# Kernel optimization log

Hardware: AMD Instinct MI355X
Metric: run time of the kernel (lower is better)

Reference implementation:

```python
import jax, jax.numpy as jnp
import numpy as np

D, H, DK, L, FF = 512, 8, 64, 6, 2048
MAXREL = 512
R = 2 * MAXREL + 1
B, S = 4, 512


def _ln(x, g, b):
    m = jnp.mean(x, -1, keepdims=True)
    v = jnp.mean((x - m) ** 2, -1, keepdims=True)
    return (x - m) * jax.lax.rsqrt(v + 1e-5) * g + b


def _gelu(x):
    return jax.nn.gelu(x, approximate=False)


def setup_inputs() -> dict:
    key = jax.random.key(0)
    ks = iter(jax.random.split(key, 64))
    def rnd(shape, scale=0.02):
        return jax.random.normal(next(ks), shape, jnp.float32) * scale
    inp = {"x": jax.random.normal(next(ks), (B, S, D), jnp.float32)}
    # SeasonalDecomposition params (3 seasonal nets stacked on leading axis)
    inp.update(
        sd_t1_w=rnd((D, D)), sd_t1_b=jnp.zeros((D,), jnp.float32),
        sd_t2_w=rnd((D, D)), sd_t2_b=jnp.zeros((D,), jnp.float32),
        sd_s1_w=rnd((3, D, D // 2)), sd_s1_b=jnp.zeros((3, D // 2), jnp.float32),
        sd_s2_w=rnd((3, D // 2, D)), sd_s2_b=jnp.zeros((3, D), jnp.float32),
        sd_r1_w=rnd((D, D // 2)), sd_r1_b=jnp.zeros((D // 2,), jnp.float32),
        sd_r2_w=rnd((D // 2, D)), sd_r2_b=jnp.zeros((D,), jnp.float32),
        sd_comb=jnp.ones((5,), jnp.float32),
        # 6 TemporalFusionTransformer layers, params stacked on leading axis L
        wq=rnd((L, D, D)), wk=rnd((L, D, D)), wv=rnd((L, D, D)),
        wo_w=rnd((L, D, D)), wo_b=jnp.zeros((L, D), jnp.float32),
        rel_k=rnd((L, R, DK), 1.0), rel_v=rnd((L, R, DK), 1.0),
        ln_attn_g=jnp.ones((L, D), jnp.float32), ln_attn_b=jnp.zeros((L, D), jnp.float32),
        ff1_w=rnd((L, D, FF)), ff1_b=jnp.zeros((L, FF), jnp.float32),
        ff2_w=rnd((L, FF, D)), ff2_b=jnp.zeros((L, D), jnp.float32),
        n1_g=jnp.ones((L, D), jnp.float32), n1_b=jnp.zeros((L, D), jnp.float32),
        n2_g=jnp.ones((L, D), jnp.float32), n2_b=jnp.zeros((L, D), jnp.float32),
    )
    return inp


def _forward(x, sd_t1_w, sd_t1_b, sd_t2_w, sd_t2_b, sd_s1_w, sd_s1_b, sd_s2_w, sd_s2_b,
             sd_r1_w, sd_r1_b, sd_r2_w, sd_r2_b, sd_comb,
             wq, wk, wv, wo_w, wo_b, rel_k, rel_v, ln_attn_g, ln_attn_b,
             ff1_w, ff1_b, ff2_w, ff2_b, n1_g, n1_b, n2_g, n2_b):
    b, s, d = x.shape
    # relative position index matrix, rp[i, j] = clip(j - i) + MAXREL
    r = jnp.arange(s)
    rp = jnp.clip(r[None, :] - r[:, None], -MAXREL, MAXREL) + MAXREL  # [S, S]

    # ---- SeasonalDecomposition (eval mode: dropout = identity) ----
    trend = _gelu(x @ sd_t1_w + sd_t1_b) @ sd_t2_w + sd_t2_b
    h = _gelu(jnp.einsum('bsd,kdm->kbsm', x, sd_s1_w) + sd_s1_b[:, None, None, :])
    seas = jnp.einsum('kbsm,kmd->kbsd', h, sd_s2_w) + sd_s2_b[:, None, None, :]  # [3,B,S,D]
    resid = _gelu(x @ sd_r1_w + sd_r1_b) @ sd_r2_w + sd_r2_b
    w = jax.nn.softmax(sd_comb)
    x = w[0] * trend + w[4] * resid + jnp.einsum('k,kbsd->bsd', w[1:4], seas)

    scale = np.float32(1.0 / np.sqrt(DK))

    def layer(xc, p):
        q = (xc @ p['wq']).reshape(b, s, H, DK).transpose(0, 2, 1, 3)  # [B,H,S,DK]
        k = (xc @ p['wk']).reshape(b, s, H, DK).transpose(0, 2, 1, 3)
        v = (xc @ p['wv']).reshape(b, s, H, DK).transpose(0, 2, 1, 3)
        scores = jnp.einsum('bhid,bhjd->bhij', q, k) * scale
        rk = p['rel_k'][rp]  # [S,S,DK] gathered rel-pos key bias
        scores = scores + jnp.einsum('bhid,ijd->bhij', q, rk)
        a = jax.nn.softmax(scores, axis=-1)
        ctx = jnp.einsum('bhij,bhjd->bhid', a, v)
        rv = p['rel_v'][rp]  # [S,S,DK]
        ctx = ctx + jnp.einsum('bhij,ijd->bhid', a, rv)
        ctx = ctx.transpose(0, 2, 1, 3).reshape(b, s, d)
        out = ctx @ p['wo_w'] + p['wo_b']
        attn = _ln(out + xc, p['ln_attn_g'], p['ln_attn_b'])
        y = _ln(xc + attn, p['n1_g'], p['n1_b'])
        ff = _gelu(y @ p['ff1_w'] + p['ff1_b']) @ p['ff2_w'] + p['ff2_b']
        y = _ln(y + ff, p['n2_g'], p['n2_b'])
        return y, None

    layers = dict(wq=wq, wk=wk, wv=wv, wo_w=wo_w, wo_b=wo_b, rel_k=rel_k, rel_v=rel_v,
                  ln_attn_g=ln_attn_g, ln_attn_b=ln_attn_b,
                  ff1_w=ff1_w, ff1_b=ff1_b, ff2_w=ff2_w, ff2_b=ff2_b,
                  n1_g=n1_g, n1_b=n1_b, n2_g=n2_g, n2_b=n2_b)
    x, _ = jax.lax.scan(layer, x, layers)
    return x


def reference(x, sd_t1_w, sd_t1_b, sd_t2_w, sd_t2_b, sd_s1_w, sd_s1_b, sd_s2_w, sd_s2_b,
              sd_r1_w, sd_r1_b, sd_r2_w, sd_r2_b, sd_comb,
              wq, wk, wv, wo_w, wo_b, rel_k, rel_v, ln_attn_g, ln_attn_b,
              ff1_w, ff1_b, ff2_w, ff2_b, n1_g, n1_b, n2_g, n2_b):
    return _forward(x, sd_t1_w, sd_t1_b, sd_t2_w, sd_t2_b, sd_s1_w, sd_s1_b, sd_s2_w, sd_s2_b,
                    sd_r1_w, sd_r1_b, sd_r2_w, sd_r2_b, sd_comb,
                    wq, wk, wv, wo_w, wo_b, rel_k, rel_v, ln_attn_g, ln_attn_b,
                    ff1_w, ff1_b, ff2_w, ff2_b, n1_g, n1_b, n2_g, n2_b)
```

## Files before the change

### kernel.cpp

```cpp
#include <hip/hip_runtime.h>
#include <hip/hip_bf16.h>

typedef __attribute__((ext_vector_type(4))) float f32x4;
typedef __attribute__((ext_vector_type(8))) short bf16x8;
typedef __attribute__((ext_vector_type(4))) short bf16x4;

#define NL 6

static __device__ __forceinline__ unsigned short f2bf(float f) {
    __hip_bfloat16 h = __float2bfloat16(f);
    return *reinterpret_cast<unsigned short*>(&h);
}
static __device__ __forceinline__ float bf2f(unsigned short u) {
    union { unsigned int u32; float f; } c; c.u32 = ((unsigned int)u) << 16; return c.f;
}
static __device__ __forceinline__ float gelu_exact(float v) {
    return 0.5f * v * (1.0f + erff(v * 0.70710678118654752f));
}
static __device__ __forceinline__ void gload_lds16(const void* g, void* l) {
    __builtin_amdgcn_global_load_lds((const __attribute__((address_space(1))) void*)g,
                                     (__attribute__((address_space(3))) void*)l, 16, 0, 0);
}
static __device__ __forceinline__ f32x4 MF(bf16x8 a, bf16x8 b, f32x4 c) {
    return __builtin_amdgcn_mfma_f32_16x16x32_bf16(a, b, c, 0, 0, 0);
}

template<int BM, int BN, bool OBF, bool BIAS, bool GACT, bool SPART, bool DUAL>
__global__ __launch_bounds__(256)
void gemm3(const unsigned short* __restrict__ A, const unsigned short* __restrict__ B,
           void* __restrict__ C, unsigned short* __restrict__ C2,
           const float* __restrict__ bias,
           int M, int N, int nkt, int skN, int lda, int ldb, int ldc, float alpha,
           int modA, long sA1, long sA2, int modB, long sB1, long sB2,
           int modC, long sC1, long sC2, int biasStride, long pStride)
{
    constexpr int MI = BM / 32, NI = BN / 32;
    constexpr int ACH = BM / 16, NCH = (BM + BN) / 16;
    __shared__ __attribute__((aligned(16))) unsigned short Ls[(BM + BN) * 32];

    const int bz = blockIdx.z;
    const int sk = SPART ? (bz % skN) : 0;
    const int z  = SPART ? (bz / skN) : bz;
    const unsigned short* Ab = A + (long)(z % modA) * sA1 + (long)(z / modA) * sA2;
    const unsigned short* Bb = B + (long)(z % modB) * sB1 + (long)(z / modB) * sB2;
    const long offC = (long)(z % modC) * sC1 + (long)(z / modC) * sC2;

    const int bm0 = blockIdx.x * BM, bn0 = blockIdx.y * BN;
    const int t = threadIdx.x, lane = t & 63, w = t >> 6;
    const int wm = (w >> 1) * (BM / 2), wn = (w & 1) * (BN / 2);
    const int crow = lane >> 2, cs = lane & 3;
    const int fr = lane & 15, kq = lane >> 4;
    const int kBase = sk * nkt * 32;

    f32x4 acc[MI][NI];
    #pragma unroll
    for (int a = 0; a < MI; a++)
        #pragma unroll
        for (int b = 0; b < NI; b++) acc[a][b] = (f32x4){0.f, 0.f, 0.f, 0.f};

    for (int kt = 0; kt < nkt; ++kt) {
        const int k0 = kBase + (kt << 5);
        #pragma unroll
        for (int c0 = 0; c0 < NCH; c0 += 4) {
            int c = c0 + w;
            if (c < NCH) {
                const unsigned short* gp;
                if (c < ACH) {
                    int rit = c * 16 + crow;
                    int ks = cs ^ (rit & 3);
                    gp = Ab + (long)(bm0 + rit) * lda + k0 + ks * 8;
                } else {
                    int rit = (c - ACH) * 16 + crow;
                    int ks = cs ^ (rit & 3);
                    gp = Bb + (long)(bn0 + rit) * ldb + k0 + ks * 8;
                }
                gload_lds16(gp, &Ls[c * 512]);
            }
        }
        __syncthreads();
        bf16x8 af[MI], bfr[NI];
        #pragma unroll
        for (int mi = 0; mi < MI; mi++) {
            int R = wm + mi * 16 + fr;
            af[mi] = *(const bf16x8*)&Ls[R * 32 + ((kq ^ (R & 3)) << 3)];
        }
        #pragma unroll
        for (int ni = 0; ni < NI; ni++) {
            int Rb = wn + ni * 16 + fr;
            bfr[ni] = *(const bf16x8*)&Ls[BM * 32 + Rb * 32 + ((kq ^ (Rb & 3)) << 3)];
        }
        #pragma unroll
        for (int mi = 0; mi < MI; mi++)
            #pragma unroll
            for (int ni = 0; ni < NI; ni++)
                acc[mi][ni] = MF(af[mi], bfr[ni], acc[mi][ni]);
        __syncthreads();
    }

    const int q4 = (lane >> 4) << 2;
    if (SPART) {
        float* P = (float*)C + sk * pStride + offC;
        #pragma unroll
        for (int mi = 0; mi < MI; mi++)
            #pragma unroll
            for (int ni = 0; ni < NI; ni++)
                #pragma unroll
                for (int j = 0; j < 4; j++) {
                    int gr = bm0 + wm + mi * 16 + q4 + j;
                    int gc = bn0 + wn + ni * 16 + fr;
                    if (gc < N) P[(long)gr * ldc + gc] = acc[mi][ni][j] * alpha;
                }
    } else {
        float* Cf = (float*)C + offC;
        unsigned short* Ch = (unsigned short*)C + offC;
        unsigned short* C2h = DUAL ? (C2 + offC) : nullptr;
        const float* bp = BIAS ? (bias + (long)z * biasStride) : nullptr;
        #pragma unroll
        for (int mi = 0; mi < MI; mi++)
            #pragma unroll
            for (int ni = 0; ni < NI; ni++)
                #pragma unroll
                for (int j = 0; j < 4; j++) {
                    int gr = bm0 + wm + mi * 16 + q4 + j;
                    int gc = bn0 + wn + ni * 16 + fr;
                    if (gc < N) {
                        float v = acc[mi][ni][j] * alpha;
                        if (BIAS) v += bp[gc];
                        if (GACT) v = gelu_exact(v);
                        if (OBF) Ch[(long)gr * ldc + gc] = f2bf(v);
                        else     Cf[(long)gr * ldc + gc] = v;
                        if (DUAL) C2h[(long)gr * ldc + gc] = f2bf(v);
                    }
                }
    }
}

__global__ __launch_bounds__(256)
void fused_attn2(const unsigned short* __restrict__ qkv,
                 const unsigned short* __restrict__ vt,
                 const unsigned short* __restrict__ rk,
                 const unsigned short* __restrict__ rvt,
                 unsigned short* __restrict__ ctx)
{
    __shared__ __attribute__((aligned(16))) unsigned short L[65536];
    const int bh = blockIdx.y, b = bh >> 3, h = bh & 7;
    const int i0 = blockIdx.x * 64;
    const int t = threadIdx.x, lane = t & 63, wv = t >> 6;
    const int crow = lane >> 2, cs = lane & 3;
    const int fr = lane & 15, kq = lane >> 4;
    const int q4 = kq << 2;
    const int iiw = wv * 16;
    const int PB = 53248, GA = 57344;

    const unsigned short* Qg = qkv + ((long)(b * 512 + i0)) * 1536 + h * 64;
    const unsigned short* Kg = qkv + ((long)(b * 512)) * 1536 + 512 + h * 64;
    const unsigned short* Vg = vt + ((long)bh * 64) * 512;

    auto stage = [&](int jt, int sbuf) {
        const int j0 = jt * 64, rbase = j0 - i0 + 448;
        const int SB = 4096 + sbuf * 24576;
        #pragma unroll
        for (int k = 0; k < 12; k++) {
            int c = wv + k * 4;
            const unsigned short* gp; int dst;
            if (c < 8) {
                int kt = c >> 2, row = (c & 3) * 16 + crow, ks = cs ^ (row & 3);
                gp = Kg + (long)(j0 + row) * 1536 + kt * 32 + ks * 8;
                dst = SB + c * 512;
            } else if (c < 16) {
                int cc = c - 8;
                int kt = cc >> 2, row = (cc & 3) * 16 + crow, ks = cs ^ (row & 3);
                gp = Vg + (long)row * 512 + j0 + kt * 32 + ks * 8;
                dst = SB + 4096 + cc * 512;
            } else if (c < 32) {
                int cc = c - 16;
                int kt = cc >> 2, row = (cc & 3) * 16 + crow, ks = cs ^ (row & 3);
                gp = rvt + (long)row * 1056 + rbase + kt * 32 + ks * 8;
                dst = SB + 8192 + cc * 512;
            } else {
                int cc = c - 32;
                int kt = cc >> 3, row = (cc & 7) * 16 + crow, ks = cs ^ (row & 3);
                gp = rk + (long)(rbase + row) * 64 + kt * 32 + ks * 8;
                dst = SB + 16384 + cc * 512;
            }
            gload_lds16(gp, &L[dst]);
        }
    };

    #pragma unroll
    for (int k = 0; k < 2; k++) {
        int c = wv + k * 4;
        int kt = c >> 2, row = (c & 3) * 16 + crow, ks = cs ^ (row & 3);
        gload_lds16(Qg + (long)row * 1536 + kt * 32 + ks * 8, &L[c * 512]);
    }
    stage(0, 0);
    __syncthreads();
    bf16x8 qf[2];
    {
        int r = iiw + fr;
        qf[0] = *(const bf16x8*)&L[r * 32 + ((kq ^ (r & 3)) << 3)];
        qf[1] = *(const bf16x8*)&L[2048 + r * 32 + ((kq ^ (r & 3)) << 3)];
    }

    f32x4 ctxa[4];
    #pragma unroll
    for (int ni = 0; ni < 4; ni++) ctxa[ni] = (f32x4){0.f, 0.f, 0.f, 0.f};
    float m_[4] = {-1e30f, -1e30f, -1e30f, -1e30f};
    float l_[4] = {0.f, 0.f, 0.f, 0.f};

    for (int jt = 0; jt < 8; ++jt) {
        const int sb = jt & 1;
        const int SB = 4096 + sb * 24576;
        if (jt < 7) stage(jt + 1, sb ^ 1);
        f32x4 gacc[8];
        #pragma unroll
        for (int wb = 0; wb < 8; wb++) {
            int Rb = wb * 16 + fr;
            bf16x8 rk0 = *(const bf16x8*)&L[SB + 16384 + Rb * 32 + ((kq ^ (Rb & 3)) << 3)];
            bf16x8 rk1 = *(const bf16x8*)&L[SB + 20480 + Rb * 32 + ((kq ^ (Rb & 3)) << 3)];
            f32x4 g = (f32x4){0.f, 0.f, 0.f, 0.f};
            g = MF(qf[0], rk0, g);
            gacc[wb] = MF(qf[1], rk1, g);
        }
        #pragma unroll
        for (int wb = 0; wb < 8; wb++)
            #pragma unroll
            for (int j = 0; j < 4; j++) {
                int il = iiw + q4 + j, ww = wb * 16 + fr;
                L[GA + il * 128 + (((ww >> 3) ^ (il & 7)) << 3) + (ww & 7)] = f2bf(gacc[wb][j]);
            }
        f32x4 s[4];
        #pragma unroll
        for (int ni = 0; ni < 4; ni++) {
            int rB = ni * 16 + fr;
            bf16x8 b0 = *(const bf16x8*)&L[SB + rB * 32 + ((kq ^ (rB & 3)) << 3)];
            bf16x8 b1 = *(const bf16x8*)&L[SB + 2048 + rB * 32 + ((kq ^ (rB & 3)) << 3)];
            f32x4 a0 = (f32x4){0.f, 0.f, 0.f, 0.f};
            a0 = MF(qf[0], b0, a0);
            s[ni] = MF(qf[1], b1, a0);
        }
        #pragma unroll
        for (int ni = 0; ni < 4; ni++)
            #pragma unroll
            for (int j = 0; j < 4; j++) {
                int il = iiw + q4 + j;
                int ww = ni * 16 + fr - il + 64;
                s[ni][j] = s[ni][j] * 0.125f
                         + bf2f(L[GA + il * 128 + (((ww >> 3) ^ (il & 7)) << 3) + (ww & 7)]);
            }
        float mx[4];
        #pragma unroll
        for (int j = 0; j < 4; j++) {
            mx[j] = fmaxf(fmaxf(s[0][j], s[1][j]), fmaxf(s[2][j], s[3][j]));
            #pragma unroll
            for (int msk = 1; msk < 16; msk <<= 1) mx[j] = fmaxf(mx[j], __shfl_xor(mx[j], msk));
        }
        float scl[4];
        #pragma unroll
        for (int j = 0; j < 4; j++) {
            float mn = fmaxf(m_[j], mx[j]);
            scl[j] = __expf(m_[j] - mn);
            m_[j] = mn;
        }
        float rs[4] = {0.f, 0.f, 0.f, 0.f};
        #pragma unroll
        for (int ni = 0; ni < 4; ni++)
            #pragma unroll
            for (int j = 0; j < 4; j++) {
                float p = __expf(s[ni][j] - m_[j]);
                s[ni][j] = p;
                rs[j] += p;
            }
        #pragma unroll
        for (int j = 0; j < 4; j++) {
            #pragma unroll
            for (int msk = 1; msk < 16; msk <<= 1) rs[j] += __shfl_xor(rs[j], msk);
            l_[j] = l_[j] * scl[j] + rs[j];
        }
        #pragma unroll
        for (int ni = 0; ni < 4; ni++)
            #pragma unroll
            for (int j = 0; j < 4; j++) ctxa[ni][j] *= scl[j];
        #pragma unroll
        for (int ni = 0; ni < 4; ni++)
            #pragma unroll
            for (int j = 0; j < 4; j++) {
                int il = iiw + q4 + j;
                int jj = ni * 16 + fr;
                unsigned short pb = f2bf(s[ni][j]);
                L[PB + il * 64 + (((jj >> 3) ^ (il & 7)) << 3) + (jj & 7)] = pb;
                int wI = jj - il + 64;
                L[GA + il * 128 + (((wI >> 3) ^ (il & 7)) << 3) + (wI & 7)] = pb;
                int wz = (wI + 64) & 127;
                L[GA + il * 128 + (((wz >> 3) ^ (il & 7)) << 3) + (wz & 7)] = 0;
            }
        const int r = iiw + fr;
        bf16x8 pa0 = *(const bf16x8*)&L[PB + r * 64 + ((kq ^ (r & 7)) << 3)];
        bf16x8 pa1 = *(const bf16x8*)&L[PB + r * 64 + (((4 + kq) ^ (r & 7)) << 3)];
        #pragma unroll
        for (int ni = 0; ni < 4; ni++) {
            int rB = ni * 16 + fr;
            bf16x8 vb0 = *(const bf16x8*)&L[SB + 4096 + rB * 32 + ((kq ^ (rB & 3)) << 3)];
            bf16x8 vb1 = *(const bf16x8*)&L[SB + 6144 + rB * 32 + ((kq ^ (rB & 3)) << 3)];
            ctxa[ni] = MF(pa0, vb0, ctxa[ni]);
            ctxa[ni] = MF(pa1, vb1, ctxa[ni]);
        }
        #pragma unroll
        for (int kt2 = 0; kt2 < 4; kt2++) {
            bf16x8 aa = *(const bf16x8*)&L[GA + r * 128 + (((kt2 * 4 + kq) ^ (r & 7)) << 3)];
            #pragma unroll
            for (int ni = 0; ni < 4; ni++) {
                int rB = ni * 16 + fr;
                bf16x8 rb = *(const bf16x8*)&L[SB + 8192 + kt2 * 2048 + rB * 32 + ((kq ^ (rB & 3)) << 3)];
                ctxa[ni] = MF(aa, rb, ctxa[ni]);
            }
        }
        __syncthreads();
    }
    #pragma unroll
    for (int j = 0; j < 4; j++) {
        float inv = 1.f / l_[j];
        int il = iiw + q4 + j;
        unsigned short* op = ctx + ((long)(b * 512 + i0 + il)) * 512 + h * 64;
        #pragma unroll
        for (int ni = 0; ni < 4; ni++)
            op[ni * 16 + fr] = f2bf(ctxa[ni][j] * inv);
    }
}

__global__ __launch_bounds__(256)
void trcast_k(const float* __restrict__ in, unsigned short* __restrict__ out,
              int R, int C, int ldo, long inStride, long outStride,
              const float* __restrict__ scp, int sczs)
{
    __shared__ unsigned short tile[32][33];
    const int z = blockIdx.z;
    const float* ip = in + (long)z * inStride;
    unsigned short* op = out + (long)z * outStride;
    const float sc = scp ? scp[z * sczs] : 1.0f;
    const int c0 = blockIdx.x * 32, r0 = blockIdx.y * 32;
    const int tx = threadIdx.x & 31, ty = threadIdx.x >> 5;
    #pragma unroll
    for (int q = 0; q < 4; q++) {
        int r = r0 + ty + q * 8;
        float v = (r < R) ? ip[(long)r * C + c0 + tx] * sc : 0.f;
        tile[ty + q * 8][tx] = f2bf(v);
    }
    __syncthreads();
    #pragma unroll
    for (int q = 0; q < 4; q++) {
        int c = c0 + ty + q * 8;
        op[(long)c * ldo + r0 + tx] = tile[tx][ty + q * 8];
    }
}

__global__ __launch_bounds__(256)
void castpad_k(const float* __restrict__ in, unsigned short* __restrict__ out,
               int R, int C, long inStride, long outStride, long nPerZ)
{
    const int z = blockIdx.z;
    for (long idx = (long)blockIdx.x * 256 + threadIdx.x; idx < nPerZ;
         idx += (long)gridDim.x * 256) {
        int r = (int)(idx / C);
        float v = (r < R) ? in[(long)z * inStride + idx] : 0.f;
        out[(long)z * outStride + idx] = f2bf(v);
    }
}

__global__ __launch_bounds__(256)
void transp_v(const unsigned short* __restrict__ v, unsigned short* __restrict__ vt, int ldv)
{
    __shared__ unsigned short tile[32][33];
    const int b = blockIdx.z;
    const int j0 = blockIdx.x * 32, c0 = blockIdx.y * 32;
    const int tx = threadIdx.x & 31, ty = threadIdx.x >> 5;
    #pragma unroll
    for (int q = 0; q < 4; q++)
        tile[ty + q * 8][tx] = v[(long)(b * 512 + j0 + ty + q * 8) * ldv + c0 + tx];
    __syncthreads();
    #pragma unroll
    for (int q = 0; q < 4; q++) {
        int c = c0 + ty + q * 8;
        int h = c >> 6, d = c & 63;
        vt[((long)(b * 8 + h) * 64 + d) * 512 + j0 + tx] = tile[tx][ty + q * 8];
    }
}

__global__ __launch_bounds__(256)
void ln2x_k(const float* __restrict__ p0, const float* __restrict__ p1,
            const float* __restrict__ wb, const float* __restrict__ x,
            const float* __restrict__ g1, const float* __restrict__ b1,
            const float* __restrict__ g2, const float* __restrict__ b2,
            float* __restrict__ yf, unsigned short* __restrict__ yb)
{
    const int wv = threadIdx.x >> 6, lane = threadIdx.x & 63;
    const long row = (long)blockIdx.x * 4 + wv;
    const int base = lane * 8;
    const float* pa = p0 + row * 512 + base;
    const float* pbp = p1 + row * 512 + base;
    const float* px = x + row * 512 + base;
    float xv[8], v[8];
    {
        float4 x0 = *(const float4*)px, x1 = *(const float4*)(px + 4);
        float4 a0 = *(const float4*)pa, a1 = *(const float4*)(pa + 4);
        float4 c0 = *(const float4*)pbp, c1 = *(const float4*)(pbp + 4);
        float4 w0 = *(const float4*)(wb + base), w1 = *(const float4*)(wb + base + 4);
        xv[0] = x0.x; xv[1] = x0.y; xv[2] = x0.z; xv[3] = x0.w;
        xv[4] = x1.x; xv[5] = x1.y; xv[6] = x1.z; xv[7] = x1.w;
        v[0] = xv[0] + a0.x + c0.x + w0.x; v[1] = xv[1] + a0.y + c0.y + w0.y;
        v[2] = xv[2] + a0.z + c0.z + w0.z; v[3] = xv[3] + a0.w + c0.w + w0.w;
        v[4] = xv[4] + a1.x + c1.x + w1.x; v[5] = xv[5] + a1.y + c1.y + w1.y;
        v[6] = xv[6] + a1.z + c1.z + w1.z; v[7] = xv[7] + a1.w + c1.w + w1.w;
    }
    float s = 0.f;
    #pragma unroll
    for (int jj = 0; jj < 8; jj++) s += v[jj];
    #pragma unroll
    for (int off = 32; off; off >>= 1) s += __shfl_xor(s, off);
    float mean = s * (1.f / 512.f);
    float vs = 0.f;
    #pragma unroll
    for (int jj = 0; jj < 8; jj++) { float d = v[jj] - mean; vs += d * d; }
    #pragma unroll
    for (int off = 32; off; off >>= 1) vs += __shfl_xor(vs, off);
    float inv = rsqrtf(vs * (1.f / 512.f) + 1e-5f);
    float4 ga = *(const float4*)(g1 + base), gb = *(const float4*)(g1 + base + 4);
    float4 ba = *(const float4*)(b1 + base), bb = *(const float4*)(b1 + base + 4);
    float gg[8] = {ga.x, ga.y, ga.z, ga.w, gb.x, gb.y, gb.z, gb.w};
    float ee[8] = {ba.x, ba.y, ba.z, ba.w, bb.x, bb.y, bb.z, bb.w};
    float tvec[8];
    #pragma unroll
    for (int jj = 0; jj < 8; jj++) tvec[jj] = xv[jj] + (v[jj] - mean) * inv * gg[jj] + ee[jj];
    float s2 = 0.f;
    #pragma unroll
    for (int jj = 0; jj < 8; jj++) s2 += tvec[jj];
    #pragma unroll
    for (int off = 32; off; off >>= 1) s2 += __shfl_xor(s2, off);
    float m2 = s2 * (1.f / 512.f);
    float vs2 = 0.f;
    #pragma unroll
    for (int jj = 0; jj < 8; jj++) { float d = tvec[jj] - m2; vs2 += d * d; }
    #pragma unroll
    for (int off = 32; off; off >>= 1) vs2 += __shfl_xor(vs2, off);
    float inv2 = rsqrtf(vs2 * (1.f / 512.f) + 1e-5f);
    float4 gc = *(const float4*)(g2 + base), gd = *(const float4*)(g2 + base + 4);
    float4 bc = *(const float4*)(b2 + base), bd = *(const float4*)(b2 + base + 4);
    float g2v[8] = {gc.x, gc.y, gc.z, gc.w, gd.x, gd.y, gd.z, gd.w};
    float b2v[8] = {bc.x, bc.y, bc.z, bc.w, bd.x, bd.y, bd.z, bd.w};
    float r[8];
    #pragma unroll
    for (int jj = 0; jj < 8; jj++) r[jj] = (tvec[jj] - m2) * inv2 * g2v[jj] + b2v[jj];
    float* pf = yf + row * 512 + base;
    *(float4*)pf = (float4){r[0], r[1], r[2], r[3]};
    *(float4*)(pf + 4) = (float4){r[4], r[5], r[6], r[7]};
    bf16x8 ov;
    #pragma unroll
    for (int jj = 0; jj < 8; jj++) ov[jj] = (short)f2bf(r[jj]);
    *(bf16x8*)(yb + row * 512 + base) = ov;
}

__global__ __launch_bounds__(256)
void lnff_k(const float* __restrict__ y1, const float* __restrict__ parts,
            const float* __restrict__ bias,
            const float* __restrict__ g, const float* __restrict__ be,
            float* __restrict__ o, unsigned short* __restrict__ ob)
{
    const int wv = threadIdx.x >> 6, lane = threadIdx.x & 63;
    const long row = (long)blockIdx.x * 4 + wv;
    const int base = lane * 8;
    const float* pa = y1 + row * 512 + base;
    float v[8];
    {
        float4 x0 = *(const float4*)pa, x1 = *(const float4*)(pa + 4);
        float4 w0 = *(const float4*)(bias + base), w1 = *(const float4*)(bias + base + 4);
        v[0] = x0.x + w0.x; v[1] = x0.y + w0.y; v[2] = x0.z + w0.z; v[3] = x0.w + w0.w;
        v[4] = x1.x + w1.x; v[5] = x1.y + w1.y; v[6] = x1.z + w1.z; v[7] = x1.w + w1.w;
    }
    #pragma unroll
    for (int k = 0; k < 4; k++) {
        const float* pp = parts + (long)k * 1048576 + row * 512 + base;
        float4 a0 = *(const float4*)pp, a1 = *(const float4*)(pp + 4);
        v[0] += a0.x; v[1] += a0.y; v[2] += a0.z; v[3] += a0.w;
        v[4] += a1.x; v[5] += a1.y; v[6] += a1.z; v[7] += a1.w;
    }
    float s = 0.f;
    #pragma unroll
    for (int jj = 0; jj < 8; jj++) s += v[jj];
    #pragma unroll
    for (int off = 32; off; off >>= 1) s += __shfl_xor(s, off);
    float mean = s * (1.f / 512.f);
    float vs = 0.f;
    #pragma unroll
    for (int jj = 0; jj < 8; jj++) { float d = v[jj] - mean; vs += d * d; }
    #pragma unroll
    for (int off = 32; off; off >>= 1) vs += __shfl_xor(vs, off);
    float inv = rsqrtf(vs * (1.f / 512.f) + 1e-5f);
    float4 g0 = *(const float4*)(g + base), g1 = *(const float4*)(g + base + 4);
    float4 e0 = *(const float4*)(be + base), e1 = *(const float4*)(be + base + 4);
    float gg[8] = {g0.x, g0.y, g0.z, g0.w, g1.x, g1.y, g1.z, g1.w};
    float ee[8] = {e0.x, e0.y, e0.z, e0.w, e1.x, e1.y, e1.z, e1.w};
    float r[8];
    #pragma unroll
    for (int jj = 0; jj < 8; jj++) r[jj] = (v[jj] - mean) * inv * gg[jj] + ee[jj];
    float* po = o + row * 512 + base;
    *(float4*)po = (float4){r[0], r[1], r[2], r[3]};
    *(float4*)(po + 4) = (float4){r[4], r[5], r[6], r[7]};
    bf16x8 ov;
    #pragma unroll
    for (int jj = 0; jj < 8; jj++) ov[jj] = (short)f2bf(r[jj]);
    *(bf16x8*)(ob + row * 512 + base) = ov;
}

__global__ void softmax5_k(const float* __restrict__ comb, float* __restrict__ c5)
{
    if (threadIdx.x == 0 && blockIdx.x == 0) {
        float c[5]; float m = -1e30f;
        for (int k = 0; k < 5; k++) { c[k] = comb[k]; m = fmaxf(m, c[k]); }
        float s = 0.f;
        for (int k = 0; k < 5; k++) { c[k] = __expf(c[k] - m); s += c[k]; }
        for (int k = 0; k < 5; k++) c5[k] = c[k] / s;
    }
}

__global__ __launch_bounds__(256)
void bias_build_k(const float* __restrict__ t1b, const float* __restrict__ r1b,
                  const float* __restrict__ s1b, const float* __restrict__ t2b,
                  const float* __restrict__ r2b, const float* __restrict__ s2b,
                  const float* __restrict__ c5, float* __restrict__ b1c,
                  float* __restrict__ bc)
{
    int i = threadIdx.x + blockIdx.x * 256;
    if (i < 512) b1c[i] = t1b[i];
    else if (i < 768) b1c[i] = r1b[i - 512];
    else if (i < 1536) b1c[i] = s1b[i - 768];
    else if (i < 2048) {
        int n = i - 1536;
        bc[n] = c5[0] * t2b[n] + c5[4] * r2b[n]
              + c5[1] * s2b[n] + c5[2] * s2b[512 + n] + c5[3] * s2b[1024 + n];
    }
}

#define G3(BM,BN,OBF,BIAS,GACT,SPART,DUAL, A,B,C,C2,bias_, M,N,NKT,SKN, lda,ldb,ldc, alpha, mA,a1,a2, mB,b1,b2, mC,c1,c2, bstr, pstr, Zg) \
    gemm3<BM,BN,OBF,BIAS,GACT,SPART,DUAL><<<dim3((M)/(BM), ((N)+(BN)-1)/(BN), (Zg)), dim3(256), 0, stream>>>( \
        (A),(B),(C),(C2),(bias_),(M),(N),(NKT),(SKN),(lda),(ldb),(ldc),(alpha), \
        (mA),(long)(a1),(long)(a2),(mB),(long)(b1),(long)(b2),(mC),(long)(c1),(long)(c2),(bstr),(long)(pstr))

extern "C" void kernel_launch(void* const* d_in, const int* in_sizes, int n_in,
                              void* d_out, int out_size, void* d_ws, size_t ws_size,
                              hipStream_t stream)
{
    (void)in_sizes; (void)n_in; (void)out_size; (void)ws_size;
    const float* x    = (const float*)d_in[0];
    const float* t1w  = (const float*)d_in[1];
    const float* t1b  = (const float*)d_in[2];
    const float* t2w  = (const float*)d_in[3];
    const float* t2b  = (const float*)d_in[4];
    const float* s1w  = (const float*)d_in[5];
    const float* s1b  = (const float*)d_in[6];
    const float* s2w  = (const float*)d_in[7];
    const float* s2b  = (const float*)d_in[8];
    const float* r1w  = (const float*)d_in[9];
    const float* r1b  = (const float*)d_in[10];
    const float* r2w  = (const float*)d_in[11];
    const float* r2b  = (const float*)d_in[12];
    const float* comb = (const float*)d_in[13];
    const float* wq   = (const float*)d_in[14];
    const float* wk   = (const float*)d_in[15];
    const float* wvv  = (const float*)d_in[16];
    const float* wow  = (const float*)d_in[17];
    const float* wob  = (const float*)d_in[18];
    const float* relk = (const float*)d_in[19];
    const float* relv = (const float*)d_in[20];
    const float* lag  = (const float*)d_in[21];
    const float* labi = (const float*)d_in[22];
    const float* f1w  = (const float*)d_in[23];
    const float* f1b  = (const float*)d_in[24];
    const float* f2w  = (const float*)d_in[25];
    const float* f2b  = (const float*)d_in[26];
    const float* n1g  = (const float*)d_in[27];
    const float* n1b  = (const float*)d_in[28];
    const float* n2g  = (const float*)d_in[29];
    const float* n2b  = (const float*)d_in[30];

    char* ws = (char*)d_ws;
    #define OFFK(kb) (ws + (size_t)(kb) * 1024)
    float* X    = (float*)OFFK(0);
    float* T3   = (float*)OFFK(8192);
    float* PART = (float*)OFFK(12288);
    unsigned short* Xb   = (unsigned short*)OFFK(45056);
    unsigned short* Xb0  = (unsigned short*)OFFK(47104);
    unsigned short* QKVb = (unsigned short*)OFFK(49152);
    unsigned short* VT   = (unsigned short*)OFFK(55296);
    unsigned short* CTXb = (unsigned short*)OFFK(57344);
    unsigned short* T3b  = (unsigned short*)OFFK(59392);
    unsigned short* FFb  = (unsigned short*)OFFK(61440);
    unsigned short* W1   = (unsigned short*)OFFK(69632);
    unsigned short* W2   = (unsigned short*)OFFK(71168);
    float* b1c = (float*)OFFK(72704);
    float* bc  = (float*)OFFK(72712);
    float* c5  = (float*)OFFK(72716);
    unsigned short* qkvT = (unsigned short*)OFFK(119808);
    unsigned short* woT  = (unsigned short*)OFFK(129024);
    unsigned short* f1wT = (unsigned short*)OFFK(132096);
    unsigned short* f2wT = (unsigned short*)OFFK(144384);
    unsigned short* relkb= (unsigned short*)OFFK(156672);
    unsigned short* rvT  = (unsigned short*)OFFK(157488);
    unsigned short* Hb   = QKVb;

    castpad_k<<<dim3(1024, 1, 1), 256, 0, stream>>>(x, Xb0, 2048, 512, 1048576, 1048576, 1048576);
    softmax5_k<<<dim3(1), 64, 0, stream>>>(comb, c5);
    bias_build_k<<<dim3(8), 256, 0, stream>>>(t1b, r1b, s1b, t2b, r2b, s2b, c5, b1c, bc);
    trcast_k<<<dim3(16, 16, 1), 256, 0, stream>>>(t1w, W1, 512, 512, 512, 0, 0, nullptr, 0);
    trcast_k<<<dim3(8, 16, 1), 256, 0, stream>>>(r1w, W1 + 262144, 512, 256, 512, 0, 0, nullptr, 0);
    trcast_k<<<dim3(8, 16, 3), 256, 0, stream>>>(s1w, W1 + 393216, 512, 256, 512, 131072, 131072, nullptr, 0);
    trcast_k<<<dim3(16, 16, 1), 256, 0, stream>>>(t2w, W2, 512, 512, 1536, 0, 0, c5, 0);
    trcast_k<<<dim3(16, 8, 1), 256, 0, stream>>>(r2w, W2 + 512, 256, 512, 1536, 0, 0, c5 + 4, 0);
    trcast_k<<<dim3(16, 8, 3), 256, 0, stream>>>(s2w, W2 + 768, 256, 512, 1536, 131072, 256, c5 + 1, 1);
    trcast_k<<<dim3(16, 16, 6), 256, 0, stream>>>(wq,  qkvT,          512, 512, 512, 262144, 786432, nullptr, 0);
    trcast_k<<<dim3(16, 16, 6), 256, 0, stream>>>(wk,  qkvT + 262144, 512, 512, 512, 262144, 786432, nullptr, 0);
    trcast_k<<<dim3(16, 16, 6), 256, 0, stream>>>(wvv, qkvT + 524288, 512, 512, 512, 262144, 786432, nullptr, 0);
    trcast_k<<<dim3(16, 16, 6), 256, 0, stream>>>(wow, woT, 512, 512, 512, 262144, 262144, nullptr, 0);
    trcast_k<<<dim3(64, 16, 6), 256, 0, stream>>>(f1w, f1wT, 512, 2048, 512, 1048576, 1048576, nullptr, 0);
    trcast_k<<<dim3(16, 64, 6), 256, 0, stream>>>(f2w, f2wT, 2048, 512, 2048, 1048576, 1048576, nullptr, 0);
    trcast_k<<<dim3(2, 33, 6), 256, 0, stream>>>(relv, rvT, 1025, 64, 1056, 65600, 67584, nullptr, 0);
    castpad_k<<<dim3(272, 1, 6), 256, 0, stream>>>(relk, relkb, 1025, 64, 65600, 69632, 69632);

    G3(128,64,true,true,true,false,false,  Xb0, W1, Hb, nullptr, b1c, 2048,1536,16,1, 512,512,1536, 1.f,
       1,0,0, 1,0,0, 1,0,0, 0,0, 1);
    G3(64,64,false,true,false,false,true, Hb, W2, X, Xb, bc, 2048,512,48,1, 1536,1536,512, 1.f,
       1,0,0, 1,0,0, 1,0,0, 0,0, 1);

    for (int l = 0; l < NL; ++l) {
        const unsigned short* qkvTl = qkvT + (long)l * 786432;
        const unsigned short* woTl  = woT + (long)l * 262144;
        const unsigned short* f1Tl  = f1wT + (long)l * 1048576;
        const unsigned short* f2Tl  = f2wT + (long)l * 1048576;
        const unsigned short* rkl   = relkb + (long)l * 69632;
        const unsigned short* rvl   = rvT + (long)l * 67584;

        G3(128,64,true,false,false,false,false, Xb, qkvTl, QKVb, nullptr, nullptr, 2048,1536,16,1, 512,512,1536, 1.f,
           1,0,0, 1,0,0, 1,0,0, 0,0, 1);
        transp_v<<<dim3(16, 16, 4), 256, 0, stream>>>(QKVb + 1024, VT, 1536);
        fused_attn2<<<dim3(8, 32), 256, 0, stream>>>(QKVb, VT, rkl, rvl, CTXb);
        G3(64,64,false,false,false,true,false, CTXb, woTl, PART, nullptr, nullptr, 2048,512,8,2, 512,512,512, 1.f,
           1,0,0, 1,0,0, 1,0,0, 0,1048576, 2);
        ln2x_k<<<dim3(512), 256, 0, stream>>>(PART, PART + 1048576, wob + l * 512, X,
                                              lag + l * 512, labi + l * 512,
                                              n1g + l * 512, n1b + l * 512, T3, T3b);
        G3(128,64,true,true,true,false,false, T3b, f1Tl, FFb, nullptr, f1b + l * 2048, 2048,2048,16,1, 512,512,2048, 1.f,
           1,0,0, 1,0,0, 1,0,0, 0,0, 1);
        G3(128,64,false,false,false,true,false, FFb, f2Tl, PART, nullptr, nullptr, 2048,512,16,4, 2048,2048,512, 1.f,
           1,0,0, 1,0,0, 1,0,0, 0,1048576, 4);
        float* outp = (l == NL - 1) ? (float*)d_out : X;
        lnff_k<<<dim3(512), 256, 0, stream>>>(T3, PART, f2b + l * 512,
                                              n2g + l * 512, n2b + l * 512, outp, Xb);
    }
}
```

Baseline: 648.0 us.

## Deepen GEMM K-tile to 64, shrink M-tiles, merge weight transposes

The GEMM kernel now stages a 64-wide K slice per iteration with an 8-way XOR swizzle and issues two MFMA k-halves per tile. This halves the number of loop iterations and barrier pairs. Several GEMM launches drop from BM=128 to BM=64 to get more blocks, and nkt is halved to match the wider K step. The four per-layer q/k/v/o weight transpose launches are merged into one kernel over 24 z-slices. In exchange, LDS per block doubles and the smaller tiles reuse each loaded operand less.

```diff
diff --git a/kernel.cpp b/kernel.cpp
--- a/kernel.cpp
+++ b/kernel.cpp
@@ -35,8 +35,8 @@
            int modC, long sC1, long sC2, int biasStride, long pStride)
 {
     constexpr int MI = BM / 32, NI = BN / 32;
-    constexpr int ACH = BM / 16, NCH = (BM + BN) / 16;
-    __shared__ __attribute__((aligned(16))) unsigned short Ls[(BM + BN) * 32];
+    constexpr int ACH = BM / 8, NCH = (BM + BN) / 8;
+    __shared__ __attribute__((aligned(16))) unsigned short Ls[(BM + BN) * 64];
 
     const int bz = blockIdx.z;
     const int sk = SPART ? (bz % skN) : 0;
@@ -48,9 +48,9 @@
     const int bm0 = blockIdx.x * BM, bn0 = blockIdx.y * BN;
     const int t = threadIdx.x, lane = t & 63, w = t >> 6;
     const int wm = (w >> 1) * (BM / 2), wn = (w & 1) * (BN / 2);
-    const int crow = lane >> 2, cs = lane & 3;
+    const int crow8 = lane >> 3, cs8 = lane & 7;
     const int fr = lane & 15, kq = lane >> 4;
-    const int kBase = sk * nkt * 32;
+    const int kBase = sk * nkt * 64;
 
     f32x4 acc[MI][NI];
     #pragma unroll
@@ -59,41 +59,45 @@
         for (int b = 0; b < NI; b++) acc[a][b] = (f32x4){0.f, 0.f, 0.f, 0.f};
 
     for (int kt = 0; kt < nkt; ++kt) {
-        const int k0 = kBase + (kt << 5);
+        const int k0 = kBase + (kt << 6);
         #pragma unroll
         for (int c0 = 0; c0 < NCH; c0 += 4) {
             int c = c0 + w;
             if (c < NCH) {
                 const unsigned short* gp;
                 if (c < ACH) {
-                    int rit = c * 16 + crow;
-                    int ks = cs ^ (rit & 3);
+                    int rit = c * 8 + crow8;
+                    int ks = cs8 ^ (rit & 7);
                     gp = Ab + (long)(bm0 + rit) * lda + k0 + ks * 8;
                 } else {
-                    int rit = (c - ACH) * 16 + crow;
-                    int ks = cs ^ (rit & 3);
+                    int rit = (c - ACH) * 8 + crow8;
+                    int ks = cs8 ^ (rit & 7);
                     gp = Bb + (long)(bn0 + rit) * ldb + k0 + ks * 8;
                 }
                 gload_lds16(gp, &Ls[c * 512]);
             }
         }
         __syncthreads();
-        bf16x8 af[MI], bfr[NI];
+        bf16x8 af[2][MI], bfr[2][NI];
         #pragma unroll
         for (int mi = 0; mi < MI; mi++) {
             int R = wm + mi * 16 + fr;
-            af[mi] = *(const bf16x8*)&Ls[R * 32 + ((kq ^ (R & 3)) << 3)];
+            af[0][mi] = *(const bf16x8*)&Ls[R * 64 + ((kq ^ (R & 7)) << 3)];
+            af[1][mi] = *(const bf16x8*)&Ls[R * 64 + (((4 + kq) ^ (R & 7)) << 3)];
         }
         #pragma unroll
         for (int ni = 0; ni < NI; ni++) {
             int Rb = wn + ni * 16 + fr;
-            bfr[ni] = *(const bf16x8*)&Ls[BM * 32 + Rb * 32 + ((kq ^ (Rb & 3)) << 3)];
-        }
-        #pragma unroll
-        for (int mi = 0; mi < MI; mi++)
-            #pragma unroll
-            for (int ni = 0; ni < NI; ni++)
-                acc[mi][ni] = MF(af[mi], bfr[ni], acc[mi][ni]);
+            bfr[0][ni] = *(const bf16x8*)&Ls[BM * 64 + Rb * 64 + ((kq ^ (Rb & 7)) << 3)];
+            bfr[1][ni] = *(const bf16x8*)&Ls[BM * 64 + Rb * 64 + (((4 + kq) ^ (Rb & 7)) << 3)];
+        }
+        #pragma unroll
+        for (int kh = 0; kh < 2; kh++)
+            #pragma unroll
+            for (int mi = 0; mi < MI; mi++)
+                #pragma unroll
+                for (int ni = 0; ni < NI; ni++)
+                    acc[mi][ni] = MF(af[kh][mi], bfr[kh][ni], acc[mi][ni]);
         __syncthreads();
     }
 
@@ -352,6 +356,30 @@
         int c = c0 + ty + q * 8;
         op[(long)c * ldo + r0 + tx] = tile[tx][ty + q * 8];
     }
+}
+
+__global__ __launch_bounds__(256)
+void qkvwo_tr(const float* __restrict__ wq, const float* __restrict__ wk,
+              const float* __restrict__ wv, const float* __restrict__ wo,
+              unsigned short* __restrict__ qkvT, unsigned short* __restrict__ woT)
+{
+    __shared__ unsigned short tile[32][33];
+    const int z = blockIdx.z;
+    const int which = z >> 1 >> 1 >> 0;
+    const int wsel = z / 6, l = z % 6;
+    const float* ip = (wsel == 0 ? wq : wsel == 1 ? wk : wsel == 2 ? wv : wo) + (long)l * 262144;
+    unsigned short* op = (wsel < 3) ? (qkvT + (long)l * 786432 + (long)wsel * 262144)
+                                    : (woT + (long)l * 262144);
+    const int c0 = blockIdx.x * 32, r0 = blockIdx.y * 32;
+    const int tx = threadIdx.x & 31, ty = threadIdx.x >> 5;
+    #pragma unroll
+    for (int q = 0; q < 4; q++)
+        tile[ty + q * 8][tx] = f2bf(ip[(long)(r0 + ty + q * 8) * 512 + c0 + tx]);
+    __syncthreads();
+    #pragma unroll
+    for (int q = 0; q < 4; q++)
+        op[(long)(c0 + ty + q * 8) * 512 + r0 + tx] = tile[tx][ty + q * 8];
+    (void)which;
 }
 
 __global__ __launch_bounds__(256)
@@ -616,18 +644,15 @@
     trcast_k<<<dim3(16, 16, 1), 256, 0, stream>>>(t2w, W2, 512, 512, 1536, 0, 0, c5, 0);
     trcast_k<<<dim3(16, 8, 1), 256, 0, stream>>>(r2w, W2 + 512, 256, 512, 1536, 0, 0, c5 + 4, 0);
     trcast_k<<<dim3(16, 8, 3), 256, 0, stream>>>(s2w, W2 + 768, 256, 512, 1536, 131072, 256, c5 + 1, 1);
-    trcast_k<<<dim3(16, 16, 6), 256, 0, stream>>>(wq,  qkvT,          512, 512, 512, 262144, 786432, nullptr, 0);
-    trcast_k<<<dim3(16, 16, 6), 256, 0, stream>>>(wk,  qkvT + 262144, 512, 512, 512, 262144, 786432, nullptr, 0);
-    trcast_k<<<dim3(16, 16, 6), 256, 0, stream>>>(wvv, qkvT + 524288, 512, 512, 512, 262144, 786432, nullptr, 0);
-    trcast_k<<<dim3(16, 16, 6), 256, 0, stream>>>(wow, woT, 512, 512, 512, 262144, 262144, nullptr, 0);
+    qkvwo_tr<<<dim3(16, 16, 24), 256, 0, stream>>>(wq, wk, wvv, wow, qkvT, woT);
     trcast_k<<<dim3(64, 16, 6), 256, 0, stream>>>(f1w, f1wT, 512, 2048, 512, 1048576, 1048576, nullptr, 0);
     trcast_k<<<dim3(16, 64, 6), 256, 0, stream>>>(f2w, f2wT, 2048, 512, 2048, 1048576, 1048576, nullptr, 0);
     trcast_k<<<dim3(2, 33, 6), 256, 0, stream>>>(relv, rvT, 1025, 64, 1056, 65600, 67584, nullptr, 0);
     castpad_k<<<dim3(272, 1, 6), 256, 0, stream>>>(relk, relkb, 1025, 64, 65600, 69632, 69632);
 
-    G3(128,64,true,true,true,false,false,  Xb0, W1, Hb, nullptr, b1c, 2048,1536,16,1, 512,512,1536, 1.f,
+    G3(64,64,true,true,true,false,false,  Xb0, W1, Hb, nullptr, b1c, 2048,1536,8,1, 512,512,1536, 1.f,
        1,0,0, 1,0,0, 1,0,0, 0,0, 1);
-    G3(64,64,false,true,false,false,true, Hb, W2, X, Xb, bc, 2048,512,48,1, 1536,1536,512, 1.f,
+    G3(64,64,false,true,false,false,true, Hb, W2, X, Xb, bc, 2048,512,24,1, 1536,1536,512, 1.f,
        1,0,0, 1,0,0, 1,0,0, 0,0, 1);
 
     for (int l = 0; l < NL; ++l) {
@@ -638,18 +663,18 @@
         const unsigned short* rkl   = relkb + (long)l * 69632;
         const unsigned short* rvl   = rvT + (long)l * 67584;
 
-        G3(128,64,true,false,false,false,false, Xb, qkvTl, QKVb, nullptr, nullptr, 2048,1536,16,1, 512,512,1536, 1.f,
+        G3(64,64,true,false,false,false,false, Xb, qkvTl, QKVb, nullptr, nullptr, 2048,1536,8,1, 512,512,1536, 1.f,
            1,0,0, 1,0,0, 1,0,0, 0,0, 1);
         transp_v<<<dim3(16, 16, 4), 256, 0, stream>>>(QKVb + 1024, VT, 1536);
         fused_attn2<<<dim3(8, 32), 256, 0, stream>>>(QKVb, VT, rkl, rvl, CTXb);
-        G3(64,64,false,false,false,true,false, CTXb, woTl, PART, nullptr, nullptr, 2048,512,8,2, 512,512,512, 1.f,
+        G3(64,64,false,false,false,true,false, CTXb, woTl, PART, nullptr, nullptr, 2048,512,4,2, 512,512,512, 1.f,
            1,0,0, 1,0,0, 1,0,0, 0,1048576, 2);
         ln2x_k<<<dim3(512), 256, 0, stream>>>(PART, PART + 1048576, wob + l * 512, X,
                                               lag + l * 512, labi + l * 512,
                                               n1g + l * 512, n1b + l * 512, T3, T3b);
-        G3(128,64,true,true,true,false,false, T3b, f1Tl, FFb, nullptr, f1b + l * 2048, 2048,2048,16,1, 512,512,2048, 1.f,
+        G3(64,64,true,true,true,false,false, T3b, f1Tl, FFb, nullptr, f1b + l * 2048, 2048,2048,8,1, 512,512,2048, 1.f,
            1,0,0, 1,0,0, 1,0,0, 0,0, 1);
-        G3(128,64,false,false,false,true,false, FFb, f2Tl, PART, nullptr, nullptr, 2048,512,16,4, 2048,2048,512, 1.f,
+        G3(64,64,false,false,false,true,false, FFb, f2Tl, PART, nullptr, nullptr, 2048,512,8,4, 2048,2048,512, 1.f,
            1,0,0, 1,0,0, 1,0,0, 0,1048576, 4);
         float* outp = (l == NL - 1) ? (float*)d_out : X;
         lnff_k<<<dim3(512), 256, 0, stream>>>(T3, PART, f2b + l * 512,
```

New measurement: 554.1 us. -14.5%, faster.
